# Kernel optimization log

Measured on AMD Instinct MI355X. Metric: run time of the kernel, lower is better.

Reference implementation:

```python
import jax, jax.numpy as jnp
import numpy as np

NUM_EMBEDDINGS = 512
EMBEDDING_DIM = 64


def setup_inputs() -> dict:
    key = jax.random.key(0)
    k1, k2 = jax.random.split(key)
    z = jax.random.normal(k1, (32, EMBEDDING_DIM, 64, 64), dtype=jnp.float32)
    lim = 1.0 / NUM_EMBEDDINGS
    emb = jax.random.uniform(k2, (NUM_EMBEDDINGS, EMBEDDING_DIM),
                             minval=-lim, maxval=lim, dtype=jnp.float32)
    return {"z": z, "emb": emb}


def reference(z, emb):
    # z: [B, C, H, W] with C == embedding_dim
    B, C, H, W = z.shape
    z_hwc = jnp.transpose(z, (0, 2, 3, 1))            # [B, H, W, C]
    flat = z_hwc.reshape(-1, C)                       # [N, C]
    dists = (jnp.sum(flat * flat, axis=1, keepdims=True)
             + jnp.sum(emb * emb, axis=1)
             - 2.0 * flat @ emb.T)                    # [N, K]
    idx = jnp.argmin(dists, axis=1)                   # [N]
    quantized = emb[idx].reshape(z_hwc.shape)         # gather == one-hot matmul
    quantized_st = z_hwc + jax.lax.stop_gradient(quantized - z_hwc)
    q_chw = jnp.transpose(quantized, (0, 3, 1, 2))    # [B, C, H, W]
    qst_chw = jnp.transpose(quantized_st, (0, 3, 1, 2))
    vq_loss = jnp.mean((jax.lax.stop_gradient(q_chw) - z) ** 2)
    commitment_loss = jnp.mean((q_chw - jax.lax.stop_gradient(z)) ** 2)
    return (qst_chw, vq_loss, commitment_loss, idx.reshape(B, H, W))
```

## Files before the change

### kernel.cpp

```cpp
#include <hip/hip_runtime.h>
#include <math.h>

#define NUM_EMB 512
#define EDIM 64
#define BATCH 32
#define HW 4096
#define NROWS (BATCH * HW)
#define NQ (NROWS * EDIM)

#define RPB 128
#define KPP 128
#define NPASS 4

#define XOFF 0
#define EOFF 8192
#define T2OFF 16384
#define T1OFF 16896
#define CBOFF 8192
#define CKOFF (8192 + 2048)
#define SFLOATS 17024

__device__ __forceinline__ float pairwise8_64(const float* v) {
    float r0 = v[0], r1 = v[1], r2 = v[2], r3 = v[3];
    float r4 = v[4], r5 = v[5], r6 = v[6], r7 = v[7];
#pragma unroll
    for (int i = 8; i < 64; i += 8) {
        r0 = __fadd_rn(r0, v[i + 0]);
        r1 = __fadd_rn(r1, v[i + 1]);
        r2 = __fadd_rn(r2, v[i + 2]);
        r3 = __fadd_rn(r3, v[i + 3]);
        r4 = __fadd_rn(r4, v[i + 4]);
        r5 = __fadd_rn(r5, v[i + 5]);
        r6 = __fadd_rn(r6, v[i + 6]);
        r7 = __fadd_rn(r7, v[i + 7]);
    }
    return __fadd_rn(__fadd_rn(__fadd_rn(r0, r1), __fadd_rn(r2, r3)),
                     __fadd_rn(__fadd_rn(r4, r5), __fadd_rn(r6, r7)));
}

__global__ void vq_prep(const float* __restrict__ emb, float* __restrict__ ws_f) {
    int k = blockIdx.x * blockDim.x + threadIdx.x;
    if (k == 0) ws_f[0] = 0.0f;
    if (k < NUM_EMB) {
        const float* e = emb + k * EDIM;
        float sq[EDIM];
#pragma unroll
        for (int c = 0; c < EDIM; ++c) sq[c] = __fmul_rn(e[c], e[c]);
        ws_f[8 + k] = pairwise8_64(sq);
    }
}

__global__ __launch_bounds__(512, 4) void vq_main(const float* __restrict__ z,
                                                  const float* __restrict__ emb,
                                                  float* __restrict__ out,
                                                  float* __restrict__ ws_f) {
    __shared__ float S[SFLOATS];
    const int tid = threadIdx.x;
    const int rt  = tid & 31;
    const int kt  = tid >> 5;
    const int row0 = rt * 4;
    const int bb  = blockIdx.x;
    const int b   = bb >> 5;
    const int hwb = (bb & 31) << 7;

    const float* zb = z + (size_t)b * (EDIM * HW) + hwb;

    {
        const int r = tid & 127, ch = tid >> 7;
#pragma unroll
        for (int j = 0; j < 16; ++j) {
            const int c = ch * 16 + j;
            S[XOFF + c * RPB + r] = zb[(size_t)c * HW + r];
        }
    }
    S[T2OFF + tid] = ws_f[8 + tid];
    __syncthreads();

    if (tid < RPB) {
        const float* xr = &S[XOFF + tid];
        float q0 = __fmul_rn(xr[0 * RPB], xr[0 * RPB]);
        float q1 = __fmul_rn(xr[1 * RPB], xr[1 * RPB]);
        float q2 = __fmul_rn(xr[2 * RPB], xr[2 * RPB]);
        float q3 = __fmul_rn(xr[3 * RPB], xr[3 * RPB]);
        float q4 = __fmul_rn(xr[4 * RPB], xr[4 * RPB]);
        float q5 = __fmul_rn(xr[5 * RPB], xr[5 * RPB]);
        float q6 = __fmul_rn(xr[6 * RPB], xr[6 * RPB]);
        float q7 = __fmul_rn(xr[7 * RPB], xr[7 * RPB]);
#pragma unroll
        for (int m = 1; m < 8; ++m) {
            float v0 = xr[(8 * m + 0) * RPB], v1 = xr[(8 * m + 1) * RPB];
            float v2 = xr[(8 * m + 2) * RPB], v3 = xr[(8 * m + 3) * RPB];
            float v4 = xr[(8 * m + 4) * RPB], v5 = xr[(8 * m + 5) * RPB];
            float v6 = xr[(8 * m + 6) * RPB], v7 = xr[(8 * m + 7) * RPB];
            q0 = __fadd_rn(q0, __fmul_rn(v0, v0));
            q1 = __fadd_rn(q1, __fmul_rn(v1, v1));
            q2 = __fadd_rn(q2, __fmul_rn(v2, v2));
            q3 = __fadd_rn(q3, __fmul_rn(v3, v3));
            q4 = __fadd_rn(q4, __fmul_rn(v4, v4));
            q5 = __fadd_rn(q5, __fmul_rn(v5, v5));
            q6 = __fadd_rn(q6, __fmul_rn(v6, v6));
            q7 = __fadd_rn(q7, __fmul_rn(v7, v7));
        }
        S[T1OFF + tid] = __fadd_rn(__fadd_rn(__fadd_rn(q0, q1), __fadd_rn(q2, q3)),
                                   __fadd_rn(__fadd_rn(q4, q5), __fadd_rn(q6, q7)));
    }
    __syncthreads();

    float t1r[4];
#pragma unroll
    for (int i = 0; i < 4; ++i) t1r[i] = S[T1OFF + row0 + i];

    float best[4];
    int   bki[4];
#pragma unroll
    for (int i = 0; i < 4; ++i) { best[i] = INFINITY; bki[i] = 0; }

    const int kb = kt * 8;

    for (int p = 0; p < NPASS; ++p) {
        {
            const int k = tid & 127, ch = tid >> 7;
            const float4* er = (const float4*)(emb + (size_t)(p * KPP + k) * EDIM);
#pragma unroll
            for (int j = 0; j < 4; ++j) {
                const float4 v = er[ch * 4 + j];
                const int c = ch * 16 + j * 4;
                S[EOFF + (c + 0) * KPP + k] = v.x;
                S[EOFF + (c + 1) * KPP + k] = v.y;
                S[EOFF + (c + 2) * KPP + k] = v.z;
                S[EOFF + (c + 3) * KPP + k] = v.w;
            }
        }
        __syncthreads();

        float acc[4][8];
#pragma unroll
        for (int i = 0; i < 4; ++i)
#pragma unroll
            for (int j = 0; j < 8; ++j) acc[i][j] = 0.0f;

#pragma unroll 4
        for (int c = 0; c < 64; ++c) {
            const float4 xa = *(const float4*)&S[XOFF + c * RPB + row0];
            const float4 e0 = *(const float4*)&S[EOFF + c * KPP + kb];
            const float4 e1 = *(const float4*)&S[EOFF + c * KPP + kb + 4];
#define ROW(i, xv) \
            acc[i][0] = __fmaf_rn(xv, e0.x, acc[i][0]); \
            acc[i][1] = __fmaf_rn(xv, e0.y, acc[i][1]); \
            acc[i][2] = __fmaf_rn(xv, e0.z, acc[i][2]); \
            acc[i][3] = __fmaf_rn(xv, e0.w, acc[i][3]); \
            acc[i][4] = __fmaf_rn(xv, e1.x, acc[i][4]); \
            acc[i][5] = __fmaf_rn(xv, e1.y, acc[i][5]); \
            acc[i][6] = __fmaf_rn(xv, e1.z, acc[i][6]); \
            acc[i][7] = __fmaf_rn(xv, e1.w, acc[i][7]);
            ROW(0, xa.x) ROW(1, xa.y) ROW(2, xa.z) ROW(3, xa.w)
#undef ROW
        }

#pragma unroll
        for (int j = 0; j < 8; ++j) {
            const int kg = p * KPP + kb + j;
            const float t2k = S[T2OFF + kg];
#pragma unroll
            for (int i = 0; i < 4; ++i) {
                float d = __fsub_rn(__fadd_rn(t1r[i], t2k),
                                    __fmul_rn(2.0f, acc[i][j]));
                if (d < best[i]) { best[i] = d; bki[i] = kg; }
            }
        }
        __syncthreads();
    }

#pragma unroll
    for (int i = 0; i < 4; ++i) {
        S[CBOFF + kt * RPB + row0 + i] = best[i];
        ((int*)S)[CKOFF + kt * RPB + row0 + i] = bki[i];
    }
    __syncthreads();

    if (tid < RPB) {
        const int row = tid;
        float B = INFINITY;
        int   K = 0;
#pragma unroll
        for (int q = 0; q < 16; ++q) {
            const float bq = S[CBOFF + q * RPB + row];
            const int   kq = ((int*)S)[CKOFF + q * RPB + row];
            if (bq < B || (bq == B && kq < K)) { B = bq; K = kq; }
        }

        const float* eb = emb + (size_t)K * EDIM;
        const float* xc = &S[XOFF + row];
        float s = 0.0f;
#pragma unroll
        for (int c = 0; c < 64; ++c) {
            const float x = xc[c * RPB];
            const float f = __fsub_rn(eb[c], x);
            out[((size_t)b * EDIM + c) * HW + hwb + row] = __fadd_rn(x, f);
            s = __fmaf_rn(f, f, s);
        }
        out[(size_t)NQ + 2 + bb * RPB + row] = (float)K;

#pragma unroll
        for (int off = 32; off > 0; off >>= 1) s += __shfl_down(s, off);
        if ((tid & 63) == 0) atomicAdd(ws_f, s);
    }
}

__global__ void vq_final(const float* __restrict__ ws_f, float* __restrict__ out) {
    float m = ws_f[0] * (1.0f / (float)NQ);
    out[NQ + 0] = m;
    out[NQ + 1] = m;
}

extern "C" void kernel_launch(void* const* d_in, const int* in_sizes, int n_in,
                              void* d_out, int out_size, void* d_ws, size_t ws_size,
                              hipStream_t stream) {
    const float* z = (const float*)d_in[0];
    const float* emb = (const float*)d_in[1];
    float* out = (float*)d_out;
    float* ws_f = (float*)d_ws;

    hipLaunchKernelGGL(vq_prep, dim3(1), dim3(512), 0, stream, emb, ws_f);
    hipLaunchKernelGGL(vq_main, dim3(NROWS / RPB), dim3(512), 0, stream, z, emb, out, ws_f);
    hipLaunchKernelGGL(vq_final, dim3(1), dim3(1), 0, stream, ws_f, out);
}
```

Measured before the change: 149.3 us.

## Use packed FP32 FMA with 2x16 register tiles and parallelize epilogue across all waves

Reworks the distance GEMM inner loop so each thread computes 2 rows by 16 codes using v_pk_fma_f32 inline asm, which halves FMA instruction count and changes the LDS load pattern. The per-block argmin reduction now merges 8 partials instead of 16. The output write and loss epilogue, previously run by only 128 threads, is spread across all 512 threads, each handling 8 channels. The trade-offs are more LDS bandwidth per FMA for the embedding operand and reliance on inline asm for packed math.

```diff
diff --git a/kernel.cpp b/kernel.cpp
--- a/kernel.cpp
+++ b/kernel.cpp
@@ -16,9 +16,13 @@
 #define EOFF 8192
 #define T2OFF 16384
 #define T1OFF 16896
-#define CBOFF 8192
-#define CKOFF (8192 + 2048)
 #define SFLOATS 17024
+
+typedef float f32x2 __attribute__((ext_vector_type(2)));
+typedef float f32x4 __attribute__((ext_vector_type(4)));
+
+#define PKFMA(ACC, X2, E2) \
+    asm("v_pk_fma_f32 %0, %1, %2, %0" : "+v"(ACC) : "v"(X2), "v"(E2))
 
 __device__ __forceinline__ float pairwise8_64(const float* v) {
     float r0 = v[0], r1 = v[1], r2 = v[2], r3 = v[3];
@@ -55,21 +59,20 @@
                                                   float* __restrict__ out,
                                                   float* __restrict__ ws_f) {
     __shared__ float S[SFLOATS];
-    const int tid = threadIdx.x;
-    const int rt  = tid & 31;
-    const int kt  = tid >> 5;
-    const int row0 = rt * 4;
-    const int bb  = blockIdx.x;
-    const int b   = bb >> 5;
-    const int hwb = (bb & 31) << 7;
+    const int tid  = threadIdx.x;
+    const int lane = tid & 63;
+    const int w    = tid >> 6;
+    const int bb   = blockIdx.x;
+    const int b    = bb >> 5;
+    const int hwb  = (bb & 31) << 7;
 
     const float* zb = z + (size_t)b * (EDIM * HW) + hwb;
 
     {
-        const int r = tid & 127, ch = tid >> 7;
+        const int r = tid & 127, cq = tid >> 7;
 #pragma unroll
         for (int j = 0; j < 16; ++j) {
-            const int c = ch * 16 + j;
+            const int c = cq * 16 + j;
             S[XOFF + c * RPB + r] = zb[(size_t)c * HW + r];
         }
     }
@@ -106,25 +109,22 @@
     }
     __syncthreads();
 
-    float t1r[4];
-#pragma unroll
-    for (int i = 0; i < 4; ++i) t1r[i] = S[T1OFF + row0 + i];
-
-    float best[4];
-    int   bki[4];
-#pragma unroll
-    for (int i = 0; i < 4; ++i) { best[i] = INFINITY; bki[i] = 0; }
-
-    const int kb = kt * 8;
-
+    const float t1lo = S[T1OFF + 2 * lane];
+    const float t1hi = S[T1OFF + 2 * lane + 1];
+
+    float best0 = INFINITY, best1 = INFINITY;
+    int   bk0 = 0, bk1 = 0;
+    const int kb = w * 16;
+
+#pragma unroll 1
     for (int p = 0; p < NPASS; ++p) {
         {
-            const int k = tid & 127, ch = tid >> 7;
-            const float4* er = (const float4*)(emb + (size_t)(p * KPP + k) * EDIM);
+            const int k = tid & 127, cq = tid >> 7;
+            const f32x4* er = (const f32x4*)(emb + (size_t)(p * KPP + k) * EDIM);
 #pragma unroll
             for (int j = 0; j < 4; ++j) {
-                const float4 v = er[ch * 4 + j];
-                const int c = ch * 16 + j * 4;
+                const f32x4 v = er[cq * 4 + j];
+                const int c = cq * 16 + j * 4;
                 S[EOFF + (c + 0) * KPP + k] = v.x;
                 S[EOFF + (c + 1) * KPP + k] = v.y;
                 S[EOFF + (c + 2) * KPP + k] = v.z;
@@ -133,78 +133,93 @@
         }
         __syncthreads();
 
-        float acc[4][8];
-#pragma unroll
-        for (int i = 0; i < 4; ++i)
-#pragma unroll
-            for (int j = 0; j < 8; ++j) acc[i][j] = 0.0f;
+        f32x2 a0[8], a1[8];
+#pragma unroll
+        for (int j = 0; j < 8; ++j) { a0[j] = (f32x2){0.f, 0.f}; a1[j] = (f32x2){0.f, 0.f}; }
 
 #pragma unroll 4
         for (int c = 0; c < 64; ++c) {
-            const float4 xa = *(const float4*)&S[XOFF + c * RPB + row0];
-            const float4 e0 = *(const float4*)&S[EOFF + c * KPP + kb];
-            const float4 e1 = *(const float4*)&S[EOFF + c * KPP + kb + 4];
-#define ROW(i, xv) \
-            acc[i][0] = __fmaf_rn(xv, e0.x, acc[i][0]); \
-            acc[i][1] = __fmaf_rn(xv, e0.y, acc[i][1]); \
-            acc[i][2] = __fmaf_rn(xv, e0.z, acc[i][2]); \
-            acc[i][3] = __fmaf_rn(xv, e0.w, acc[i][3]); \
-            acc[i][4] = __fmaf_rn(xv, e1.x, acc[i][4]); \
-            acc[i][5] = __fmaf_rn(xv, e1.y, acc[i][5]); \
-            acc[i][6] = __fmaf_rn(xv, e1.z, acc[i][6]); \
-            acc[i][7] = __fmaf_rn(xv, e1.w, acc[i][7]);
-            ROW(0, xa.x) ROW(1, xa.y) ROW(2, xa.z) ROW(3, xa.w)
-#undef ROW
+            const f32x2 xv = *(const f32x2*)&S[XOFF + c * RPB + 2 * lane];
+            const f32x4 ea = *(const f32x4*)&S[EOFF + c * KPP + kb];
+            const f32x4 eb = *(const f32x4*)&S[EOFF + c * KPP + kb + 4];
+            const f32x4 ec = *(const f32x4*)&S[EOFF + c * KPP + kb + 8];
+            const f32x4 ed = *(const f32x4*)&S[EOFF + c * KPP + kb + 12];
+            const f32x2 e0 = __builtin_shufflevector(ea, ea, 0, 1);
+            const f32x2 e1 = __builtin_shufflevector(ea, ea, 2, 3);
+            const f32x2 e2 = __builtin_shufflevector(eb, eb, 0, 1);
+            const f32x2 e3 = __builtin_shufflevector(eb, eb, 2, 3);
+            const f32x2 e4 = __builtin_shufflevector(ec, ec, 0, 1);
+            const f32x2 e5 = __builtin_shufflevector(ec, ec, 2, 3);
+            const f32x2 e6 = __builtin_shufflevector(ed, ed, 0, 1);
+            const f32x2 e7 = __builtin_shufflevector(ed, ed, 2, 3);
+            const f32x2 x0 = __builtin_shufflevector(xv, xv, 0, 0);
+            const f32x2 x1 = __builtin_shufflevector(xv, xv, 1, 1);
+            PKFMA(a0[0], x0, e0); PKFMA(a0[1], x0, e1);
+            PKFMA(a0[2], x0, e2); PKFMA(a0[3], x0, e3);
+            PKFMA(a0[4], x0, e4); PKFMA(a0[5], x0, e5);
+            PKFMA(a0[6], x0, e6); PKFMA(a0[7], x0, e7);
+            PKFMA(a1[0], x1, e0); PKFMA(a1[1], x1, e1);
+            PKFMA(a1[2], x1, e2); PKFMA(a1[3], x1, e3);
+            PKFMA(a1[4], x1, e4); PKFMA(a1[5], x1, e5);
+            PKFMA(a1[6], x1, e6); PKFMA(a1[7], x1, e7);
         }
 
 #pragma unroll
         for (int j = 0; j < 8; ++j) {
-            const int kg = p * KPP + kb + j;
-            const float t2k = S[T2OFF + kg];
-#pragma unroll
-            for (int i = 0; i < 4; ++i) {
-                float d = __fsub_rn(__fadd_rn(t1r[i], t2k),
-                                    __fmul_rn(2.0f, acc[i][j]));
-                if (d < best[i]) { best[i] = d; bki[i] = kg; }
-            }
+            const int kg = p * KPP + kb + 2 * j;
+            const float t2lo = S[T2OFF + kg];
+            const float t2hi = S[T2OFF + kg + 1];
+            float d;
+            d = __fsub_rn(__fadd_rn(t1lo, t2lo), __fmul_rn(2.0f, a0[j].x));
+            if (d < best0) { best0 = d; bk0 = kg; }
+            d = __fsub_rn(__fadd_rn(t1lo, t2hi), __fmul_rn(2.0f, a0[j].y));
+            if (d < best0) { best0 = d; bk0 = kg + 1; }
+            d = __fsub_rn(__fadd_rn(t1hi, t2lo), __fmul_rn(2.0f, a1[j].x));
+            if (d < best1) { best1 = d; bk1 = kg; }
+            d = __fsub_rn(__fadd_rn(t1hi, t2hi), __fmul_rn(2.0f, a1[j].y));
+            if (d < best1) { best1 = d; bk1 = kg + 1; }
         }
         __syncthreads();
     }
 
-#pragma unroll
-    for (int i = 0; i < 4; ++i) {
-        S[CBOFF + kt * RPB + row0 + i] = best[i];
-        ((int*)S)[CKOFF + kt * RPB + row0 + i] = bki[i];
-    }
+    S[EOFF + w * RPB + 2 * lane]     = best0;
+    S[EOFF + w * RPB + 2 * lane + 1] = best1;
+    ((int*)S)[EOFF + 1024 + w * RPB + 2 * lane]     = bk0;
+    ((int*)S)[EOFF + 1024 + w * RPB + 2 * lane + 1] = bk1;
     __syncthreads();
 
     if (tid < RPB) {
-        const int row = tid;
         float B = INFINITY;
         int   K = 0;
 #pragma unroll
-        for (int q = 0; q < 16; ++q) {
-            const float bq = S[CBOFF + q * RPB + row];
-            const int   kq = ((int*)S)[CKOFF + q * RPB + row];
+        for (int q = 0; q < 8; ++q) {
+            const float bq = S[EOFF + q * RPB + tid];
+            const int   kq = ((int*)S)[EOFF + 1024 + q * RPB + tid];
             if (bq < B || (bq == B && kq < K)) { B = bq; K = kq; }
         }
-
-        const float* eb = emb + (size_t)K * EDIM;
-        const float* xc = &S[XOFF + row];
-        float s = 0.0f;
-#pragma unroll
-        for (int c = 0; c < 64; ++c) {
-            const float x = xc[c * RPB];
-            const float f = __fsub_rn(eb[c], x);
-            out[((size_t)b * EDIM + c) * HW + hwb + row] = __fadd_rn(x, f);
+        ((int*)S)[T1OFF + tid] = K;
+        out[(size_t)NQ + 2 + bb * RPB + tid] = (float)K;
+    }
+    __syncthreads();
+
+    float s = 0.0f;
+#pragma unroll
+    for (int h = 0; h < 2; ++h) {
+        const int rr = h * 64 + lane;
+        const int K  = ((int*)S)[T1OFF + rr];
+        const float* ebp = emb + (size_t)K * EDIM;
+#pragma unroll
+        for (int j = 0; j < 8; ++j) {
+            const int c = w * 8 + j;
+            const float x = S[XOFF + c * RPB + rr];
+            const float f = __fsub_rn(ebp[c], x);
+            out[((size_t)b * EDIM + c) * HW + hwb + rr] = __fadd_rn(x, f);
             s = __fmaf_rn(f, f, s);
         }
-        out[(size_t)NQ + 2 + bb * RPB + row] = (float)K;
-
-#pragma unroll
-        for (int off = 32; off > 0; off >>= 1) s += __shfl_down(s, off);
-        if ((tid & 63) == 0) atomicAdd(ws_f, s);
-    }
+    }
+#pragma unroll
+    for (int off = 32; off > 0; off >>= 1) s += __shfl_down(s, off);
+    if (lane == 0) atomicAdd(ws_f, s);
 }
 
 __global__ void vq_final(const float* __restrict__ ws_f, float* __restrict__ out) {
```

After: 189.1 us. 26.7% more time.
